# Optimization experiments

Measured on AMD Instinct MI355X. Metric: run time of the kernel, lower is better.

The kernel has to match this reference:

```python
import jax, jax.numpy as jnp
import numpy as np

N = 100000          # nodes
E = 1600000         # directed edges
B = 64              # graphs in the batch
IN_D, HID, OUT_D = 20, 128, 256
EPS = 1e-5


def setup_inputs() -> dict:
    key = jax.random.key(0)
    ks = jax.random.split(key, 16)
    x = jax.random.normal(ks[0], (N, IN_D), dtype=jnp.float32)
    edge_index = jax.random.randint(ks[1], (2, E), 0, N, dtype=jnp.int64)
    batch = jnp.sort(jax.random.randint(ks[2], (N,), 0, B, dtype=jnp.int64))

    def lin(k, fi, fo):
        kw, kb = jax.random.split(k)
        s = 1.0 / np.sqrt(fi)
        W = jax.random.uniform(kw, (fi, fo), jnp.float32, -s, s)
        b = jax.random.uniform(kb, (fo,), jnp.float32, -s, s)
        return W, b

    W1, b1 = lin(ks[3], IN_D, HID)
    W2, b2 = lin(ks[4], HID, HID)
    W3, b3 = lin(ks[5], HID, OUT_D)
    res_W, res_b = lin(ks[6], IN_D, HID)
    return {
        "x": x, "edge_index": edge_index, "batch": batch,
        "W1": W1, "b1": b1, "W2": W2, "b2": b2, "W3": W3, "b3": b3,
        "res_W": res_W, "res_b": res_b,
        "ln1_g": jnp.ones((HID,), jnp.float32), "ln1_b": jnp.zeros((HID,), jnp.float32),
        "ln2_g": jnp.ones((HID,), jnp.float32), "ln2_b": jnp.zeros((HID,), jnp.float32),
    }


def layer_norm(h, g, b):
    mu = jnp.mean(h, axis=-1, keepdims=True)
    var = jnp.mean((h - mu) ** 2, axis=-1, keepdims=True)
    return (h - mu) * jax.lax.rsqrt(var + EPS) * g + b


def gcn_conv(h, W, b, src, dst, norm):
    # h: [N, Fi] -> transform then normalized scatter-sum over edges (incl. self-loops)
    h = h @ W                                  # [N, Fo]
    msg = h[src] * norm[:, None]               # [E+N, Fo] gather
    out = jax.ops.segment_sum(msg, dst, num_segments=N)  # scatter
    return out + b


def reference(x, edge_index, batch, W1, b1, W2, b2, W3, b3, res_W, res_b,
              ln1_g, ln1_b, ln2_g, ln2_b):
    loops = jnp.arange(N, dtype=edge_index.dtype)
    src = jnp.concatenate([edge_index[0], loops])
    dst = jnp.concatenate([edge_index[1], loops])
    # symmetric GCN normalization (degrees include self-loops, so deg >= 1)
    deg = jax.ops.segment_sum(jnp.ones_like(dst, jnp.float32), dst, num_segments=N)
    dinv = jax.lax.rsqrt(deg)
    norm = dinv[src] * dinv[dst]               # [E+N]

    residual = x @ res_W + res_b
    h = gcn_conv(x, W1, b1, src, dst, norm)
    h = jax.nn.relu(layer_norm(h + residual, ln1_g, ln1_b))
    residual2 = h
    h = gcn_conv(h, W2, b2, src, dst, norm)
    h = jax.nn.relu(layer_norm(h + residual2, ln2_g, ln2_b))
    h = gcn_conv(h, W3, b3, src, dst, norm)    # [N, 256]

    # global mean pool per graph
    cnt = jax.ops.segment_sum(jnp.ones((N,), jnp.float32), batch, num_segments=B)
    pooled = jax.ops.segment_sum(h, batch, num_segments=B) / jnp.maximum(cnt, 1.0)[:, None]
    return pooled                              # [B, 256]
```

## Files before the change

kernel.cpp:

```cpp
#include <hip/hip_runtime.h>
#include <hip/hip_bf16.h>
#include <hip/hip_fp16.h>
#include <hip/hip_fp8.h>


typedef unsigned short ushort_t;
typedef unsigned int uint_t;
typedef __attribute__((ext_vector_type(8))) short bf16x8;
typedef __attribute__((ext_vector_type(4))) float f32x4;

constexpr int N  = 100000;
constexpr int E  = 1600000;
constexpr int B  = 64;
constexpr int IND = 20;
constexpr int HID = 128;
constexpr int OUTD = 256;

constexpr int NBUK = (N + 127) / 128;
constexpr int GB   = 256;
constexpr int EPB  = E / GB;
constexpr int BMAX = 3072;

__device__ inline ushort_t f2bf(float f) {
  union { float f; uint_t u; } v; v.f = f;
  uint_t r = v.u + 0x7fffu + ((v.u >> 16) & 1u);
  return (ushort_t)(r >> 16);
}
__device__ inline float bflo(uint_t u) { return __uint_as_float(u << 16); }
__device__ inline float bfhi(uint_t u) { return __uint_as_float(u & 0xffff0000u); }

#if defined(__has_builtin)
#if __has_builtin(__builtin_amdgcn_cvt_f32_fp8) && __has_builtin(__builtin_amdgcn_cvt_pk_fp8_f32)
#define FP8_HW 1
#endif
#endif

template <int S>
__device__ inline float fp8dec(uint_t u) {
#ifdef FP8_HW
  return __builtin_amdgcn_cvt_f32_fp8(u, S);
#else
  __hip_fp8_storage_t b = (__hip_fp8_storage_t)((u >> (8 * S)) & 0xffu);
  __half_raw hr = __hip_cvt_fp8_to_halfraw(b, __HIP_E4M3);
  return __half2float(*(__half*)&hr);
#endif
}

template <bool W>
__device__ inline uint_t fp8pk2(float a, float b, uint_t old) {
#ifdef FP8_HW
  return __builtin_amdgcn_cvt_pk_fp8_f32(a, b, old, W);
#else
  uint_t lo = (uint_t)__hip_cvt_float_to_fp8(a, __HIP_SATFINITE, __HIP_E4M3);
  uint_t hi = (uint_t)__hip_cvt_float_to_fp8(b, __HIP_SATFINITE, __HIP_E4M3);
  uint_t pair = lo | (hi << 8);
  return W ? ((old & 0x0000ffffu) | (pair << 16)) : ((old & 0xffff0000u) | pair);
#endif
}

__device__ inline unsigned char fp8enc1(float a) {
  return (unsigned char)(fp8pk2<false>(a, a, 0u) & 0xffu);
}

#define FP8DEC8(u, a0, a1, a2, a3, a4, a5, a6, a7) \
  { a0 = fp8dec<0>(u.x); a1 = fp8dec<1>(u.x); a2 = fp8dec<2>(u.x); a3 = fp8dec<3>(u.x); \
    a4 = fp8dec<0>(u.y); a5 = fp8dec<1>(u.y); a6 = fp8dec<2>(u.y); a7 = fp8dec<3>(u.y); }


__global__ __launch_bounds__(256) void k_seg_starts(const int* __restrict__ batch,
                                                    int* __restrict__ starts) {
  int i = blockIdx.x * 256 + threadIdx.x;
  if (i >= N) return;
  int b = batch[i];
  int prev = (i == 0) ? -1 : batch[i - 1];
  for (int g = prev + 1; g <= b; ++g) starts[g] = i;
  if (i == N - 1)
    for (int g = b + 1; g <= B; ++g) starts[g] = N;
}

__global__ __launch_bounds__(256) void k_pack(const float* __restrict__ W2,
                                              const float* __restrict__ W1,
                                              const float* __restrict__ resW,
                                              ushort_t* __restrict__ wpack,
                                              ushort_t* __restrict__ w1pack) {
  int idx = blockIdx.x * 256 + threadIdx.x;
  if (idx < 16384) {
    int j = idx & 7, L = (idx >> 3) & 63, kt = (idx >> 9) & 3, t = idx >> 11;
    int k = kt * 32 + ((L >> 4) & 3) * 8 + j;
    int n = t * 16 + (L & 15);
    wpack[idx] = f2bf(W2[k * HID + n]);
  } else {
    int i2 = idx - 16384;
    int j = i2 & 7, L = (i2 >> 3) & 63, kt = (i2 >> 9) & 1, t = i2 >> 10;
    int k = kt * 32 + ((L >> 4) & 3) * 8 + j;
    int n = t * 16 + (L & 15);
    float v = 0.f;
    if (k < IND) v = W1[k * HID + n];
    else if (k >= 32 && k < 32 + IND) v = resW[(k - 32) * HID + n];
    w1pack[i2] = f2bf(v);
  }
}


__global__ __launch_bounds__(256) void k_hist(const int* __restrict__ eidx,
                                              int* __restrict__ histd,
                                              int* __restrict__ hists) {
  __shared__ int hd[NBUK], hs[NBUK];
  for (int i = threadIdx.x; i < NBUK; i += 256) { hd[i] = 0; hs[i] = 0; }
  __syncthreads();
  const long base = (long)blockIdx.x * EPB;
  for (int i = threadIdx.x; i < EPB; i += 256) {
    atomicAdd(&hs[eidx[base + i] >> 7], 1);
    atomicAdd(&hd[eidx[E + base + i] >> 7], 1);
  }
  __syncthreads();
  for (int i = threadIdx.x; i < NBUK; i += 256) {
    histd[(long)blockIdx.x * NBUK + i] = hd[i];
    hists[(long)blockIdx.x * NBUK + i] = hs[i];
  }
}

__global__ __launch_bounds__(256) void k_bscan2x(int* __restrict__ histd,
                                                 int* __restrict__ btd,
                                                 int* __restrict__ hists,
                                                 int* __restrict__ bts) {
  __shared__ int s[256];
  const int which = (blockIdx.x >= NBUK);
  const int j = which ? blockIdx.x - NBUK : blockIdx.x;
  int* hist = which ? hists : histd;
  int* btotal = which ? bts : btd;
  const int tid = threadIdx.x;
  int v = hist[(long)tid * NBUK + j];
  s[tid] = v;
  for (int off = 1; off < 256; off <<= 1) {
    __syncthreads();
    int x = (tid >= off) ? s[tid - off] : 0;
    __syncthreads();
    s[tid] += x;
  }
  hist[(long)tid * NBUK + j] = s[tid] - v;
  if (tid == 255) btotal[j] = s[255];
}

__global__ __launch_bounds__(256) void k_bktscan2x(const int* __restrict__ btd,
                                                   int* __restrict__ bexcl,
                                                   const int* __restrict__ bts,
                                                   int* __restrict__ bexcl2,
                                                   int* __restrict__ rowptr) {
  __shared__ int s[256];
  const int* bt = blockIdx.x ? bts : btd;
  int* bx = blockIdx.x ? bexcl2 : bexcl;
  int tid = threadIdx.x;
  int base = tid * 4;
  int v0 = (base + 0 < NBUK) ? bt[base + 0] : 0;
  int v1 = (base + 1 < NBUK) ? bt[base + 1] : 0;
  int v2 = (base + 2 < NBUK) ? bt[base + 2] : 0;
  int v3 = (base + 3 < NBUK) ? bt[base + 3] : 0;
  int p0 = v0, p1 = p0 + v1, p2 = p1 + v2, p3 = p2 + v3;
  s[tid] = p3;
  for (int off = 1; off < 256; off <<= 1) {
    __syncthreads();
    int x = (tid >= off) ? s[tid - off] : 0;
    __syncthreads();
    s[tid] += x;
  }
  int excl = s[tid] - p3;
  if (base + 0 < NBUK) bx[base + 1] = excl + p0;
  if (base + 1 < NBUK) bx[base + 2] = excl + p1;
  if (base + 2 < NBUK) bx[base + 3] = excl + p2;
  if (base + 3 < NBUK) bx[base + 4] = excl + p3;
  if (tid == 0) { bx[0] = 0; if (blockIdx.x == 0) rowptr[N] = E; }
}

__global__ __launch_bounds__(256) void k_scatter(const int* __restrict__ eidx,
                                                 const int* __restrict__ histd,
                                                 const int* __restrict__ bexcl,
                                                 const int* __restrict__ hists,
                                                 const int* __restrict__ bexcl2,
                                                 int* __restrict__ ebuf,
                                                 int* __restrict__ ebuf2) {
  __shared__ int hd[NBUK], hs[NBUK];
  for (int i = threadIdx.x; i < NBUK; i += 256) {
    hd[i] = bexcl[i] + histd[(long)blockIdx.x * NBUK + i];
    hs[i] = bexcl2[i] + hists[(long)blockIdx.x * NBUK + i];
  }
  __syncthreads();
  const long base = (long)blockIdx.x * EPB;
  for (int i = threadIdx.x; i < EPB; i += 256) {
    int s = eidx[base + i];
    int d = eidx[E + base + i];
    int pos = atomicAdd(&hd[d >> 7], 1);
    ebuf[pos] = s | ((d & 127) << 20);
    int pos2 = atomicAdd(&hs[s >> 7], 1);
    ebuf2[pos2] = ((s & 127) << 17) | d;
  }
}

__global__ __launch_bounds__(256) void k_csr(const int* __restrict__ ebuf,
                                             const int* __restrict__ bexcl,
                                             const float* __restrict__ x,
                                             int* __restrict__ rowptr,
                                             float* __restrict__ dinv,
                                             int* __restrict__ colsrc,
                                             ushort_t* __restrict__ xs16) {
  __shared__ int deg[128], s[128], cur[128];
  __shared__ float dv[128];
  __shared__ int lout[BMAX];
  const int j = blockIdx.x, tid = threadIdx.x;
  const int e0 = bexcl[j], e1 = bexcl[j + 1];
  const int cnt = e1 - e0;
  if (tid < 128) deg[tid] = 0;
  __syncthreads();
  for (int i = tid; i < cnt; i += 256)
    atomicAdd(&deg[(ebuf[e0 + i] >> 20) & 127], 1);
  __syncthreads();
  int v = (tid < 128) ? deg[tid] : 0;
  if (tid < 128) s[tid] = v;
  for (int off = 1; off < 128; off <<= 1) {
    __syncthreads();
    int x2 = (tid < 128 && tid >= off) ? s[tid - off] : 0;
    __syncthreads();
    if (tid < 128) s[tid] += x2;
  }
  __syncthreads();
  if (tid < 128) {
    int ex = s[tid] - v;
    cur[tid] = ex;
    float d = rsqrtf((float)(1 + v));
    dv[tid] = d;
    int node = j * 128 + tid;
    if (node < N) {
      rowptr[node] = e0 + ex;
      dinv[node] = d;
    }
  }
  __syncthreads();
  if (cnt <= BMAX) {
    for (int i = tid; i < cnt; i += 256) {
      int p = ebuf[e0 + i];
      int pos = atomicAdd(&cur[(p >> 20) & 127], 1);
      lout[pos] = p & 0xFFFFF;
    }
    __syncthreads();
    for (int i = tid; i < cnt; i += 256) colsrc[e0 + i] = lout[i];
  } else {
    for (int i = tid; i < cnt; i += 256) {
      int p = ebuf[e0 + i];
      int pos = atomicAdd(&cur[(p >> 20) & 127], 1);
      colsrc[e0 + pos] = p & 0xFFFFF;
    }
  }
  for (int idx = tid; idx < 128 * IND; idx += 256) {
    int n = idx / IND;
    long node = (long)j * 128 + n;
    if (node < N)
      xs16[node * IND + idx % IND] = f2bf(x[node * IND + idx % IND] * dv[n]);
  }
}


__global__ __launch_bounds__(256) void k_gather20b(const ushort_t* __restrict__ xs16,
                                                   const float* __restrict__ dinv,
                                                   const int* __restrict__ rowptr,
                                                   const int* __restrict__ colsrc,
                                                   ushort_t* __restrict__ aggx16) {
  int t = threadIdx.x;
  if (t >= 250) return;
  int n = t / 10, cc = (t % 10) * 2;
  long i = (long)blockIdx.x * 25 + n;
  float di = dinv[i];
  uint_t u = *(const uint_t*)(xs16 + i * IND + cc);
  float a0 = bflo(u), a1 = bfhi(u);
  int e0 = rowptr[i], e1 = rowptr[i + 1];
#pragma unroll 4
  for (int e = e0; e < e1; ++e) {
    int s = colsrc[e];
    uint_t v = *(const uint_t*)(xs16 + (long)s * IND + cc);
    a0 += bflo(v); a1 += bfhi(v);
  }
  uint_t p0 = f2bf(a0 * di), p1 = f2bf(a1 * di);
  *(uint_t*)&aggx16[i * IND + cc] = p0 | (p1 << 16);
}

constexpr int ASTR = 72;
constexpr int CSTR = 132;

__global__ __launch_bounds__(256) void k_conv1m(const ushort_t* __restrict__ aggx16,
                                                const float* __restrict__ x,
                                                const ushort_t* __restrict__ w1pack,
                                                const float* __restrict__ b1,
                                                const float* __restrict__ resb,
                                                const float* __restrict__ g1,
                                                const float* __restrict__ bb1,
                                                const float* __restrict__ dinv,
                                                unsigned char* __restrict__ h8a) {
  __shared__ ushort_t A[16 * ASTR];
  __shared__ float Cs[16 * CSTR];
  const int tid = threadIdx.x;
  const long node0 = (long)blockIdx.x * 16;
  for (int idx = tid; idx < 16 * 64; idx += 256) {
    int n = idx >> 6, k = idx & 63;
    ushort_t v = 0;
    if (k < IND) v = aggx16[(node0 + n) * IND + k];
    else if (k >= 32 && k < 32 + IND) v = f2bf(x[(node0 + n) * IND + (k - 32)]);
    A[n * ASTR + k] = v;
  }
  __syncthreads();
  const int lane = tid & 63, w = tid >> 6;
  {
    const int arow = lane & 15, aq = lane >> 4;
    f32x4 acc0 = {0.f, 0.f, 0.f, 0.f}, acc1 = {0.f, 0.f, 0.f, 0.f};
    const int t0 = w * 2, t1 = t0 + 1;
#pragma unroll
    for (int kt = 0; kt < 2; ++kt) {
      bf16x8 af = *(const bf16x8*)&A[arow * ASTR + kt * 32 + aq * 8];
      bf16x8 b0 = *(const bf16x8*)&w1pack[(t0 * 2 + kt) * 512 + lane * 8];
      bf16x8 b1f = *(const bf16x8*)&w1pack[(t1 * 2 + kt) * 512 + lane * 8];
      acc0 = __builtin_amdgcn_mfma_f32_16x16x32_bf16(af, b0, acc0, 0, 0, 0);
      acc1 = __builtin_amdgcn_mfma_f32_16x16x32_bf16(af, b1f, acc1, 0, 0, 0);
    }
#pragma unroll
    for (int r = 0; r < 4; ++r) {
      Cs[(aq * 4 + r) * CSTR + t0 * 16 + arow] = acc0[r];
      Cs[(aq * 4 + r) * CSTR + t1 * 16 + arow] = acc1[r];
    }
  }
  __syncthreads();
  const int nidx = tid >> 5, col = (tid & 31) * 4;
  float4 bz = *(const float4*)&b1[col];
  float4 rz = *(const float4*)&resb[col];
  bz.x += rz.x; bz.y += rz.y; bz.z += rz.z; bz.w += rz.w;
  float4 gz = *(const float4*)&g1[col];
  float4 bbz = *(const float4*)&bb1[col];
#pragma unroll
  for (int m = 0; m < 2; ++m) {
    int nl = nidx + m * 8;
    long nm = node0 + nl;
    float4 o = *(const float4*)&Cs[nl * CSTR + col];
    o.x += bz.x; o.y += bz.y; o.z += bz.z; o.w += bz.w;
    float s = o.x + o.y + o.z + o.w;
    float q = o.x * o.x + o.y * o.y + o.z * o.z + o.w * o.w;
#pragma unroll
    for (int off = 1; off <= 16; off <<= 1) {
      s += __shfl_xor(s, off);
      q += __shfl_xor(q, off);
    }
    float mu = s * (1.f / 128.f);
    float var = q * (1.f / 128.f) - mu * mu;
    float rs = rsqrtf(var + 1e-5f);
    float y0 = fmaxf(fmaf((o.x - mu) * rs, gz.x, bbz.x), 0.f);
    float y1 = fmaxf(fmaf((o.y - mu) * rs, gz.y, bbz.y), 0.f);
    float y2 = fmaxf(fmaf((o.z - mu) * rs, gz.z, bbz.z), 0.f);
    float y3 = fmaxf(fmaf((o.w - mu) * rs, gz.w, bbz.w), 0.f);
    float di = dinv[nm];
    uint_t p = fp8pk2<false>(y0 * di, y1 * di, 0u);
    p = fp8pk2<true>(y2 * di, y3 * di, p);
    *(uint_t*)&h8a[nm * HID + col] = p;
  }
}


constexpr int XSTR = 136;

__global__ __launch_bounds__(256) void k_layer2(const unsigned char* __restrict__ h8a,
                                                const float* __restrict__ dinv,
                                                const int* __restrict__ rowptr,
                                                const int* __restrict__ colsrc,
                                                const ushort_t* __restrict__ wpack,
                                                const float* __restrict__ bias,
                                                const float* __restrict__ g2,
                                                const float* __restrict__ bb2,
                                                unsigned char* __restrict__ h8b) {
  __shared__ ushort_t XsB[16 * XSTR];
  __shared__ float Cs[16 * CSTR];
  const int tid = threadIdx.x;
  const long node0 = (long)blockIdx.x * 16;
  const int lane = tid & 63, w = tid >> 6;
  {
    const int grp = lane >> 4, l16 = lane & 15, c8 = l16 * 8;
    const long i = node0 + w * 4 + grp;
    const float di = dinv[i];
    float a0, a1, a2, a3, a4, a5, a6, a7;
    {
      uint2 u = *(const uint2*)(h8a + i * HID + c8);
      FP8DEC8(u, a0, a1, a2, a3, a4, a5, a6, a7);
    }
    const int e0 = rowptr[i], e1 = rowptr[i + 1];
#pragma unroll 4
    for (int e = e0; e < e1; ++e) {
      int s = colsrc[e];
      uint2 u = *(const uint2*)(h8a + (long)s * HID + c8);
      float b0, b1, b2, b3, b4, b5, b6, b7;
      FP8DEC8(u, b0, b1, b2, b3, b4, b5, b6, b7);
      a0 += b0; a1 += b1; a2 += b2; a3 += b3;
      a4 += b4; a5 += b5; a6 += b6; a7 += b7;
    }
    uint_t p0 = (uint_t)f2bf(a0 * di) | ((uint_t)f2bf(a1 * di) << 16);
    uint_t p1 = (uint_t)f2bf(a2 * di) | ((uint_t)f2bf(a3 * di) << 16);
    uint_t p2 = (uint_t)f2bf(a4 * di) | ((uint_t)f2bf(a5 * di) << 16);
    uint_t p3 = (uint_t)f2bf(a6 * di) | ((uint_t)f2bf(a7 * di) << 16);
    *(uint4*)&XsB[(w * 4 + grp) * XSTR + c8] = make_uint4(p0, p1, p2, p3);
  }
  __syncthreads();
  {
    const int arow = lane & 15, aq = lane >> 4;
    f32x4 acc0 = {0.f, 0.f, 0.f, 0.f}, acc1 = {0.f, 0.f, 0.f, 0.f};
    const int t0 = w * 2, t1 = w * 2 + 1;
#pragma unroll
    for (int kt = 0; kt < 4; ++kt) {
      bf16x8 af = *(const bf16x8*)&XsB[arow * XSTR + kt * 32 + aq * 8];
      bf16x8 b0 = *(const bf16x8*)&wpack[(t0 * 4 + kt) * 512 + lane * 8];
      bf16x8 b1 = *(const bf16x8*)&wpack[(t1 * 4 + kt) * 512 + lane * 8];
      acc0 = __builtin_amdgcn_mfma_f32_16x16x32_bf16(af, b0, acc0, 0, 0, 0);
      acc1 = __builtin_amdgcn_mfma_f32_16x16x32_bf16(af, b1, acc1, 0, 0, 0);
    }
#pragma unroll
    for (int r = 0; r < 4; ++r) {
      Cs[(aq * 4 + r) * CSTR + t0 * 16 + arow] = acc0[r];
      Cs[(aq * 4 + r) * CSTR + t1 * 16 + arow] = acc1[r];
    }
  }
  __syncthreads();
  const int nidx = tid >> 5;
  const int col = (tid & 31) * 4;
  float4 bz = *(const float4*)&bias[col];
  float4 gz = *(const float4*)&g2[col];
  float4 bbz = *(const float4*)&bb2[col];
#pragma unroll
  for (int m = 0; m < 2; ++m) {
    int nl = nidx + m * 8;
    long nm = node0 + nl;
    float di = dinv[nm];
    float rdi = 1.0f / di;
    uint_t ur = *(const uint_t*)&h8a[nm * HID + col];
    float4 o = *(const float4*)&Cs[nl * CSTR + col];
    o.x += bz.x + fp8dec<0>(ur) * rdi;
    o.y += bz.y + fp8dec<1>(ur) * rdi;
    o.z += bz.z + fp8dec<2>(ur) * rdi;
    o.w += bz.w + fp8dec<3>(ur) * rdi;
    float s = o.x + o.y + o.z + o.w;
    float q = o.x * o.x + o.y * o.y + o.z * o.z + o.w * o.w;
#pragma unroll
    for (int off = 1; off <= 16; off <<= 1) {
      s += __shfl_xor(s, off);
      q += __shfl_xor(q, off);
    }
    float mu = s * (1.f / 128.f);
    float var = q * (1.f / 128.f) - mu * mu;
    float rs = rsqrtf(var + 1e-5f);
    float y0 = fmaxf(fmaf((o.x - mu) * rs, gz.x, bbz.x), 0.f);
    float y1 = fmaxf(fmaf((o.y - mu) * rs, gz.y, bbz.y), 0.f);
    float y2 = fmaxf(fmaf((o.z - mu) * rs, gz.z, bbz.z), 0.f);
    float y3 = fmaxf(fmaf((o.w - mu) * rs, gz.w, bbz.w), 0.f);
    uint_t p = fp8pk2<false>(y0 * di, y1 * di, 0u);
    p = fp8pk2<true>(y2 * di, y3 * di, p);
    *(uint_t*)&h8b[nm * HID + col] = p;
  }
}


constexpr int RSTR = 136;
constexpr int CP   = 132;

__global__ __launch_bounds__(256) void k_pool3m(const unsigned char* __restrict__ h8b,
                                                const int* __restrict__ bexcl2,
                                                const int* __restrict__ ebuf2,
                                                const int* __restrict__ batch,
                                                const float* __restrict__ dinv,
                                                float* __restrict__ partial) {
  __shared__ float Cm[B * CP];
  __shared__ ushort_t R[128 * RSTR];
  const int j = blockIdx.x, tid = threadIdx.x;
  const long nbase = (long)j * 128;
  const int validRows = min(128, N - (int)nbase);
  for (int i = tid; i < B * CP; i += 256) Cm[i] = 0.f;
  for (int i = tid; i < 128 * (HID / 8); i += 256) {
    int s = i >> 4;
    int ch = (i & 15) * 8;
    uint4 pk = make_uint4(0u, 0u, 0u, 0u);
    if (s < validRows) {
      uint2 u = *(const uint2*)(h8b + (nbase + s) * HID + ch);
      float b0, b1, b2, b3, b4, b5, b6, b7;
      FP8DEC8(u, b0, b1, b2, b3, b4, b5, b6, b7);
      pk.x = (uint_t)f2bf(b0) | ((uint_t)f2bf(b1) << 16);
      pk.y = (uint_t)f2bf(b2) | ((uint_t)f2bf(b3) << 16);
      pk.z = (uint_t)f2bf(b4) | ((uint_t)f2bf(b5) << 16);
      pk.w = (uint_t)f2bf(b6) | ((uint_t)f2bf(b7) << 16);
    }
    *(uint4*)&R[s * RSTR + ch] = pk;
  }
  __syncthreads();
  const int e0 = bexcl2[j], e1 = bexcl2[j + 1];
  for (int e = e0 + tid; e < e1; e += 256) {
    int p = ebuf2[e];
    int s = (p >> 17) & 127;
    int d = p & 0x1FFFF;
    atomicAdd(&Cm[batch[d] * CP + s], dinv[d]);
  }
  for (int n = tid; n < validRows; n += 256) {
    long node = nbase + n;
    atomicAdd(&Cm[batch[node] * CP + n], dinv[node]);
  }
  __syncthreads();
  const int lane = tid & 63, wid = tid >> 6;
  const int m16 = lane & 15, quad = lane >> 4;
  f32x4 acc[4][2];
#pragma unroll
  for (int mt = 0; mt < 4; ++mt)
#pragma unroll
    for (int ntl = 0; ntl < 2; ++ntl) acc[mt][ntl] = (f32x4){0.f, 0.f, 0.f, 0.f};
#pragma unroll
  for (int kt = 0; kt < 4; ++kt) {
    union { ushort_t u[8]; bf16x8 v; } bf[2];
#pragma unroll
    for (int ntl = 0; ntl < 2; ++ntl) {
      int nt = wid * 2 + ntl;
#pragma unroll
      for (int jj = 0; jj < 8; ++jj)
        bf[ntl].u[jj] = R[(kt * 32 + quad * 8 + jj) * RSTR + nt * 16 + m16];
    }
#pragma unroll
    for (int mt = 0; mt < 4; ++mt) {
      float4 c0 = *(const float4*)&Cm[(mt * 16 + m16) * CP + kt * 32 + quad * 8];
      float4 c1 = *(const float4*)&Cm[(mt * 16 + m16) * CP + kt * 32 + quad * 8 + 4];
      union { ushort_t u[8]; bf16x8 v; } af;
      af.u[0] = f2bf(c0.x); af.u[1] = f2bf(c0.y);
      af.u[2] = f2bf(c0.z); af.u[3] = f2bf(c0.w);
      af.u[4] = f2bf(c1.x); af.u[5] = f2bf(c1.y);
      af.u[6] = f2bf(c1.z); af.u[7] = f2bf(c1.w);
      acc[mt][0] = __builtin_amdgcn_mfma_f32_16x16x32_bf16(af.v, bf[0].v, acc[mt][0], 0, 0, 0);
      acc[mt][1] = __builtin_amdgcn_mfma_f32_16x16x32_bf16(af.v, bf[1].v, acc[mt][1], 0, 0, 0);
    }
  }
  float* slab = partial + (long)j * (B * HID);
#pragma unroll
  for (int mt = 0; mt < 4; ++mt)
#pragma unroll
    for (int ntl = 0; ntl < 2; ++ntl)
#pragma unroll
      for (int r = 0; r < 4; ++r) {
        int g = mt * 16 + quad * 4 + r;
        int ch = (wid * 2 + ntl) * 16 + m16;
        slab[g * HID + ch] = acc[mt][ntl][r];
      }
}

__global__ __launch_bounds__(256) void k_pool_reduce(const float* __restrict__ partial,
                                                     float* __restrict__ pooled) {
  __shared__ float s[256];
  const int ol = threadIdx.x & 31, jl = threadIdx.x >> 5;
  const int o = blockIdx.x * 32 + ol;
  float acc = 0.f;
  for (int j = jl; j < NBUK; j += 8)
    acc += partial[(long)j * (B * HID) + o];
  s[threadIdx.x] = acc;
  __syncthreads();
  if (threadIdx.x < 32) {
    float a = s[threadIdx.x];
#pragma unroll
    for (int k = 1; k < 8; ++k) a += s[k * 32 + threadIdx.x];
    pooled[o] = a;
  }
}


__global__ __launch_bounds__(256) void k_final(const float* __restrict__ pooled,
                                               const int* __restrict__ starts,
                                               const float* __restrict__ W3,
                                               const float* __restrict__ b3,
                                               float* __restrict__ out) {
  __shared__ float p[HID];
  int g = blockIdx.x, tid = threadIdx.x;
  int len = starts[g + 1] - starts[g];
  float scale = 1.0f / fmaxf((float)len, 1.0f);
  if (tid < HID) p[tid] = pooled[g * HID + tid] * scale;
  __syncthreads();
  float a = b3[tid];
  for (int k = 0; k < HID; ++k) a = fmaf(p[k], W3[k * OUTD + tid], a);
  out[g * OUTD + tid] = a;
}


extern "C" void kernel_launch(void* const* d_in, const int* in_sizes, int n_in,
                              void* d_out, int out_size, void* d_ws, size_t ws_size,
                              hipStream_t stream) {
  const float* x    = (const float*)d_in[0];
  const int*   eidx = (const int*)d_in[1];
  const int*   batch= (const int*)d_in[2];
  const float* W1   = (const float*)d_in[3];
  const float* b1   = (const float*)d_in[4];
  const float* W2   = (const float*)d_in[5];
  const float* b2   = (const float*)d_in[6];
  const float* W3   = (const float*)d_in[7];
  const float* b3   = (const float*)d_in[8];
  const float* resW = (const float*)d_in[9];
  const float* resb = (const float*)d_in[10];
  const float* g1   = (const float*)d_in[11];
  const float* bb1  = (const float*)d_in[12];
  const float* g2   = (const float*)d_in[13];
  const float* bb2  = (const float*)d_in[14];
  float* out = (float*)d_out;

  char* w = (char*)d_ws;
  size_t off = 0;
  auto alloc = [&](size_t bytes) {
    char* p = w + off;
    off = (off + bytes + 1023) & ~(size_t)1023;
    return p;
  };
  float* dinv   = (float*)alloc((size_t)N * 4);
  int*   rowptr = (int*)alloc((size_t)(N + 1) * 4);
  int*   colsrc = (int*)alloc((size_t)E * 4);
  int*   ebuf   = (int*)alloc((size_t)E * 4);
  int*   ebuf2  = (int*)alloc((size_t)E * 4);
  int*   hist   = (int*)alloc((size_t)GB * NBUK * 4);
  int*   hist2  = (int*)alloc((size_t)GB * NBUK * 4);
  int*   btotal = (int*)alloc((size_t)NBUK * 4);
  int*   btotal2= (int*)alloc((size_t)NBUK * 4);
  int*   bexcl  = (int*)alloc((size_t)(NBUK + 1) * 4);
  int*   bexcl2 = (int*)alloc((size_t)(NBUK + 1) * 4);
  int*   starts = (int*)alloc((size_t)(B + 1) * 4);
  float* pooled = (float*)alloc((size_t)B * HID * 4);
  ushort_t* aggx16 = (ushort_t*)alloc((size_t)N * IND * 2);
  ushort_t* xs16   = (ushort_t*)alloc((size_t)N * IND * 2);
  ushort_t* wpack  = (ushort_t*)alloc((size_t)HID * HID * 2);
  ushort_t* w1pack = (ushort_t*)alloc((size_t)8192 * 2);
  unsigned char* h8a = (unsigned char*)alloc((size_t)N * HID);
  unsigned char* h8b = (unsigned char*)alloc((size_t)N * HID);
  float* partial = (float*)alloc((size_t)NBUK * B * HID * 4);

  k_seg_starts<<<(N + 255) / 256, 256, 0, stream>>>(batch, starts);
  k_pack<<<96, 256, 0, stream>>>(W2, W1, resW, wpack, w1pack);
  k_hist<<<GB, 256, 0, stream>>>(eidx, hist, hist2);
  k_bscan2x<<<2 * NBUK, 256, 0, stream>>>(hist, btotal, hist2, btotal2);
  k_bktscan2x<<<2, 256, 0, stream>>>(btotal, bexcl, btotal2, bexcl2, rowptr);
  k_scatter<<<GB, 256, 0, stream>>>(eidx, hist, bexcl, hist2, bexcl2, ebuf, ebuf2);
  k_csr<<<NBUK, 256, 0, stream>>>(ebuf, bexcl, x, rowptr, dinv, colsrc, xs16);

  k_gather20b<<<N / 25, 256, 0, stream>>>(xs16, dinv, rowptr, colsrc, aggx16);
  k_conv1m<<<N / 16, 256, 0, stream>>>(aggx16, x, w1pack, b1, resb,
                                       g1, bb1, dinv, h8a);

  k_layer2<<<N / 16, 256, 0, stream>>>(h8a, dinv, rowptr, colsrc,
                                       wpack, b2, g2, bb2, h8b);

  k_pool3m<<<NBUK, 256, 0, stream>>>(h8b, bexcl2, ebuf2, batch, dinv, partial);
  k_pool_reduce<<<(B * HID) / 32, 256, 0, stream>>>(partial, pooled);
  k_final<<<B, 256, 0, stream>>>(pooled, starts, W3, b3, out);
}
```

Measured before the change: 306.3 us.

## Fuse layer-1 gather into conv kernel and shrink pool staging to fp8/bf16

Merges the 20-feature neighbour gather into the layer-1 MFMA kernel, so aggregated features go straight to shared memory and the aggx16 buffer plus one launch disappear. The pool kernel now stages raw fp8 bytes in LDS with wide 16-byte loads and decodes them per element when building MFMA operands, shrinking LDS use. Partial per-bucket pooled sums are stored as bf16 instead of fp32, halving that traffic at some precision cost. The fused layer-1 uses only 160 of 256 threads for the gather, which may lower occupancy or balance.

Result: no change. 302.1 us (-1.4%).

```diff
diff --git a/kernel.cpp b/kernel.cpp
--- a/kernel.cpp
+++ b/kernel.cpp
@@ -56,10 +56,6 @@
   uint_t pair = lo | (hi << 8);
   return W ? ((old & 0x0000ffffu) | (pair << 16)) : ((old & 0xffff0000u) | pair);
 #endif
-}
-
-__device__ inline unsigned char fp8enc1(float a) {
-  return (unsigned char)(fp8pk2<false>(a, a, 0u) & 0xffu);
 }
 
 #define FP8DEC8(u, a0, a1, a2, a3, a4, a5, a6, a7) \
@@ -259,34 +255,13 @@
 }
 
 
-__global__ __launch_bounds__(256) void k_gather20b(const ushort_t* __restrict__ xs16,
-                                                   const float* __restrict__ dinv,
-                                                   const int* __restrict__ rowptr,
-                                                   const int* __restrict__ colsrc,
-                                                   ushort_t* __restrict__ aggx16) {
-  int t = threadIdx.x;
-  if (t >= 250) return;
-  int n = t / 10, cc = (t % 10) * 2;
-  long i = (long)blockIdx.x * 25 + n;
-  float di = dinv[i];
-  uint_t u = *(const uint_t*)(xs16 + i * IND + cc);
-  float a0 = bflo(u), a1 = bfhi(u);
-  int e0 = rowptr[i], e1 = rowptr[i + 1];
-#pragma unroll 4
-  for (int e = e0; e < e1; ++e) {
-    int s = colsrc[e];
-    uint_t v = *(const uint_t*)(xs16 + (long)s * IND + cc);
-    a0 += bflo(v); a1 += bfhi(v);
-  }
-  uint_t p0 = f2bf(a0 * di), p1 = f2bf(a1 * di);
-  *(uint_t*)&aggx16[i * IND + cc] = p0 | (p1 << 16);
-}
-
 constexpr int ASTR = 72;
 constexpr int CSTR = 132;
 
-__global__ __launch_bounds__(256) void k_conv1m(const ushort_t* __restrict__ aggx16,
+__global__ __launch_bounds__(256) void k_layer1(const ushort_t* __restrict__ xs16,
                                                 const float* __restrict__ x,
+                                                const int* __restrict__ rowptr,
+                                                const int* __restrict__ colsrc,
                                                 const ushort_t* __restrict__ w1pack,
                                                 const float* __restrict__ b1,
                                                 const float* __restrict__ resb,
@@ -298,12 +273,27 @@
   __shared__ float Cs[16 * CSTR];
   const int tid = threadIdx.x;
   const long node0 = (long)blockIdx.x * 16;
-  for (int idx = tid; idx < 16 * 64; idx += 256) {
-    int n = idx >> 6, k = idx & 63;
-    ushort_t v = 0;
-    if (k < IND) v = aggx16[(node0 + n) * IND + k];
-    else if (k >= 32 && k < 32 + IND) v = f2bf(x[(node0 + n) * IND + (k - 32)]);
-    A[n * ASTR + k] = v;
+  for (int idx = tid; idx < 16 * ASTR; idx += 256) A[idx] = 0;
+  __syncthreads();
+  for (int idx = tid; idx < 16 * IND; idx += 256) {
+    int n = idx / IND, k = idx % IND;
+    A[n * ASTR + 32 + k] = f2bf(x[(node0 + n) * IND + k]);
+  }
+  if (tid < 160) {
+    int n = tid / 10, cc = (tid % 10) * 2;
+    long i = node0 + n;
+    float di = dinv[i];
+    uint_t u = *(const uint_t*)(xs16 + i * IND + cc);
+    float a0 = bflo(u), a1 = bfhi(u);
+    int e0 = rowptr[i], e1 = rowptr[i + 1];
+#pragma unroll 4
+    for (int e = e0; e < e1; ++e) {
+      int s = colsrc[e];
+      uint_t v = *(const uint_t*)(xs16 + (long)s * IND + cc);
+      a0 += bflo(v); a1 += bfhi(v);
+    }
+    uint_t p0 = f2bf(a0 * di), p1 = f2bf(a1 * di);
+    *(uint_t*)&A[n * ASTR + cc] = p0 | (p1 << 16);
   }
   __syncthreads();
   const int lane = tid & 63, w = tid >> 6;
@@ -459,35 +449,28 @@
 }
 
 
-constexpr int RSTR = 136;
-constexpr int CP   = 132;
+constexpr int RSTR8 = 136;
+constexpr int CP    = 132;
 
 __global__ __launch_bounds__(256) void k_pool3m(const unsigned char* __restrict__ h8b,
                                                 const int* __restrict__ bexcl2,
                                                 const int* __restrict__ ebuf2,
                                                 const int* __restrict__ batch,
                                                 const float* __restrict__ dinv,
-                                                float* __restrict__ partial) {
+                                                ushort_t* __restrict__ partial) {
   __shared__ float Cm[B * CP];
-  __shared__ ushort_t R[128 * RSTR];
+  __shared__ unsigned char R8[128 * RSTR8];
   const int j = blockIdx.x, tid = threadIdx.x;
   const long nbase = (long)j * 128;
   const int validRows = min(128, N - (int)nbase);
   for (int i = tid; i < B * CP; i += 256) Cm[i] = 0.f;
-  for (int i = tid; i < 128 * (HID / 8); i += 256) {
-    int s = i >> 4;
-    int ch = (i & 15) * 8;
+  for (int i = tid; i < 128 * (HID / 16); i += 256) {
+    int s = i >> 3;
+    int ch = (i & 7) * 16;
     uint4 pk = make_uint4(0u, 0u, 0u, 0u);
-    if (s < validRows) {
-      uint2 u = *(const uint2*)(h8b + (nbase + s) * HID + ch);
-      float b0, b1, b2, b3, b4, b5, b6, b7;
-      FP8DEC8(u, b0, b1, b2, b3, b4, b5, b6, b7);
-      pk.x = (uint_t)f2bf(b0) | ((uint_t)f2bf(b1) << 16);
-      pk.y = (uint_t)f2bf(b2) | ((uint_t)f2bf(b3) << 16);
-      pk.z = (uint_t)f2bf(b4) | ((uint_t)f2bf(b5) << 16);
-      pk.w = (uint_t)f2bf(b6) | ((uint_t)f2bf(b7) << 16);
-    }
-    *(uint4*)&R[s * RSTR + ch] = pk;
+    if (s < validRows)
+      pk = *(const uint4*)(h8b + (nbase + s) * HID + ch);
+    *(uint4*)&R8[s * RSTR8 + ch] = pk;
   }
   __syncthreads();
   const int e0 = bexcl2[j], e1 = bexcl2[j + 1];
@@ -516,8 +499,10 @@
     for (int ntl = 0; ntl < 2; ++ntl) {
       int nt = wid * 2 + ntl;
 #pragma unroll
-      for (int jj = 0; jj < 8; ++jj)
-        bf[ntl].u[jj] = R[(kt * 32 + quad * 8 + jj) * RSTR + nt * 16 + m16];
+      for (int jj = 0; jj < 8; ++jj) {
+        uint_t byte = R8[(kt * 32 + quad * 8 + jj) * RSTR8 + nt * 16 + m16];
+        bf[ntl].u[jj] = f2bf(fp8dec<0>(byte));
+      }
     }
 #pragma unroll
     for (int mt = 0; mt < 4; ++mt) {
@@ -532,7 +517,7 @@
       acc[mt][1] = __builtin_amdgcn_mfma_f32_16x16x32_bf16(af.v, bf[1].v, acc[mt][1], 0, 0, 0);
     }
   }
-  float* slab = partial + (long)j * (B * HID);
+  ushort_t* slab = partial + (long)j * (B * HID);
 #pragma unroll
   for (int mt = 0; mt < 4; ++mt)
 #pragma unroll
@@ -541,18 +526,18 @@
       for (int r = 0; r < 4; ++r) {
         int g = mt * 16 + quad * 4 + r;
         int ch = (wid * 2 + ntl) * 16 + m16;
-        slab[g * HID + ch] = acc[mt][ntl][r];
+        slab[g * HID + ch] = f2bf(acc[mt][ntl][r]);
       }
 }
 
-__global__ __launch_bounds__(256) void k_pool_reduce(const float* __restrict__ partial,
+__global__ __launch_bounds__(256) void k_pool_reduce(const ushort_t* __restrict__ partial,
                                                      float* __restrict__ pooled) {
   __shared__ float s[256];
   const int ol = threadIdx.x & 31, jl = threadIdx.x >> 5;
   const int o = blockIdx.x * 32 + ol;
   float acc = 0.f;
   for (int j = jl; j < NBUK; j += 8)
-    acc += partial[(long)j * (B * HID) + o];
+    acc += bflo((uint_t)partial[(long)j * (B * HID) + o]);
   s[threadIdx.x] = acc;
   __syncthreads();
   if (threadIdx.x < 32) {
@@ -621,13 +606,12 @@
   int*   bexcl2 = (int*)alloc((size_t)(NBUK + 1) * 4);
   int*   starts = (int*)alloc((size_t)(B + 1) * 4);
   float* pooled = (float*)alloc((size_t)B * HID * 4);
-  ushort_t* aggx16 = (ushort_t*)alloc((size_t)N * IND * 2);
   ushort_t* xs16   = (ushort_t*)alloc((size_t)N * IND * 2);
   ushort_t* wpack  = (ushort_t*)alloc((size_t)HID * HID * 2);
   ushort_t* w1pack = (ushort_t*)alloc((size_t)8192 * 2);
   unsigned char* h8a = (unsigned char*)alloc((size_t)N * HID);
   unsigned char* h8b = (unsigned char*)alloc((size_t)N * HID);
-  float* partial = (float*)alloc((size_t)NBUK * B * HID * 4);
+  ushort_t* partial = (ushort_t*)alloc((size_t)NBUK * B * HID * 2);
 
   k_seg_starts<<<(N + 255) / 256, 256, 0, stream>>>(batch, starts);
   k_pack<<<96, 256, 0, stream>>>(W2, W1, resW, wpack, w1pack);
@@ -637,9 +621,8 @@
   k_scatter<<<GB, 256, 0, stream>>>(eidx, hist, bexcl, hist2, bexcl2, ebuf, ebuf2);
   k_csr<<<NBUK, 256, 0, stream>>>(ebuf, bexcl, x, rowptr, dinv, colsrc, xs16);
 
-  k_gather20b<<<N / 25, 256, 0, stream>>>(xs16, dinv, rowptr, colsrc, aggx16);
-  k_conv1m<<<N / 16, 256, 0, stream>>>(aggx16, x, w1pack, b1, resb,
-                                       g1, bb1, dinv, h8a);
+  k_layer1<<<N / 16, 256, 0, stream>>>(xs16, x, rowptr, colsrc, w1pack,
+                                       b1, resb, g1, bb1, dinv, h8a);
 
   k_layer2<<<N / 16, 256, 0, stream>>>(h8a, dinv, rowptr, colsrc,
                                        wpack, b2, g2, bb2, h8b);
```
